# Kernel tuning notes

Hardware: AMD Instinct MI355X
Metric: run time of the kernel (lower is better)

## Reference

```python
import jax, jax.numpy as jnp
import numpy as np

N_NODES = 50000
N_EDGES = 800000
IN_C = 128
OUT_C = 128
ALPHA = 0.2  # leaky_relu negative slope (args.egat_alpha)
EDGE_K = 3   # edgefeat width, fixed by W_out in-dim = 3*out_channels


def setup_inputs() -> dict:
    key = jax.random.key(0)
    k = jax.random.split(key, 7)
    h = jax.random.normal(k[0], (N_NODES, IN_C), dtype=jnp.float32)
    edge_index = jax.random.randint(k[1], (2, N_EDGES), 0, N_NODES, dtype=jnp.int64)
    edgefeat = jax.random.uniform(k[2], (N_EDGES, EDGE_K), dtype=jnp.float32)
    # glorot-initialized linear weights (stored as [in, out] for x @ W)
    def glorot(kk, fan_in, fan_out):
        lim = jnp.sqrt(6.0 / (fan_in + fan_out)).astype(jnp.float32)
        return jax.random.uniform(kk, (fan_in, fan_out), jnp.float32, -lim, lim)
    W = glorot(k[3], IN_C, OUT_C)
    a1 = glorot(k[4], OUT_C, 1)
    a2 = glorot(k[5], OUT_C, 1)
    W_out = glorot(k[6], EDGE_K * OUT_C, OUT_C)
    return {"h": h, "edge_index": edge_index, "edgefeat": edgefeat,
            "W": W, "a1": a1, "a2": a2, "W_out": W_out}


def reference(h, edge_index, edgefeat, W, a1, a2, W_out):
    src = edge_index[0]  # j: message source
    dst = edge_index[1]  # i: aggregation target
    n = h.shape[0]

    Wh = h @ W                                   # [N, C]
    s1 = Wh @ a1                                 # [N, 1] alpha_j scores
    s2 = Wh @ a2                                 # [N, 1] alpha_i scores

    # edge_update: leaky_relu(alpha_j + alpha_i) * edge_attr, then edge softmax over dst
    e = s1[src] + s2[dst]                        # [E, 1]
    e = jnp.where(e >= 0, e, ALPHA * e)
    alpha = e * edgefeat                         # [E, 3]
    m = jax.ops.segment_max(alpha, dst, num_segments=n)      # [N, 3]
    m = jnp.where(jnp.isfinite(m), m, 0.0)
    ex = jnp.exp(alpha - m[dst])
    denom = jax.ops.segment_sum(ex, dst, num_segments=n)     # [N, 3]
    att = ex / (denom[dst] + 1e-16)              # [E, 3] (dropout p applied at eval -> identity)

    # message: outer product att[E,3] x x_j[E,C] -> [E, 3C] -> W_out -> [E, C]
    x_j = Wh[src]                                # [E, C]
    msg = (att[:, :, None] * x_j[:, None, :]).reshape(att.shape[0], EDGE_K * Wh.shape[1])
    msg = msg @ W_out                            # [E, C]

    # aggregate: sum at destination nodes
    out = jax.ops.segment_sum(msg, dst, num_segments=n)      # [N, C]
    return out
```

## Files before the change

kernel.cpp:

```cpp
#include <hip/hip_runtime.h>
#include <hip/hip_bf16.h>

#define ALPHA 0.2f
typedef unsigned int uint32;
typedef __attribute__((ext_vector_type(8))) short short8;
typedef __attribute__((ext_vector_type(4))) float f32x4;

static __device__ __forceinline__ unsigned short f2bf(float f) {
    unsigned int u = __float_as_uint(f);
    u += 0x7fffu + ((u >> 16) & 1u);
    return (unsigned short)(u >> 16);
}
static __device__ __forceinline__ uint32 pk2bf(float lo, float hi) {
    return (uint32)f2bf(lo) | ((uint32)f2bf(hi) << 16);
}
static __device__ __forceinline__ float bflo(uint32 u) { return __uint_as_float(u << 16); }
static __device__ __forceinline__ float bfhi(uint32 u) { return __uint_as_float(u & 0xffff0000u); }

__global__ __launch_bounds__(256) void k1_hist_prep(const int* __restrict__ ei,
                                                    int* __restrict__ counts,
                                                    int* __restrict__ eslot, int E,
                                                    const float* __restrict__ W,
                                                    const float* __restrict__ Wout,
                                                    const float* __restrict__ a1,
                                                    const float* __restrict__ a2,
                                                    unsigned short* __restrict__ WBT,
                                                    unsigned short* __restrict__ WoutT,
                                                    float* __restrict__ w1f,
                                                    float* __restrict__ w2f, int nbh) {
    const int tid = threadIdx.x;
    if ((int)blockIdx.x < nbh) {
        int e = blockIdx.x * 256 + tid;
        if (e < E) eslot[e] = atomicAdd(&counts[ei[E + e]], 1);
        return;
    }
    int bp = blockIdx.x - nbh;
    if (bp < 8) {
        for (int n = bp * 16; n < bp * 16 + 16; ++n)
            for (int c = tid; c < 128; c += 256)
                WBT[n * 128 + c] = f2bf(W[c * 128 + n]);
    } else if (bp < 24) {
        int q = bp - 8;
        for (int n = q * 8; n < q * 8 + 8; ++n)
            for (int c = tid; c < 384; c += 256)
                WoutT[n * 384 + c] = f2bf(Wout[c * 128 + n]);
    } else {
        if (tid < 128) {
            float acc1 = 0.f, acc2 = 0.f;
            for (int c = 0; c < 128; ++c) {
                float w = W[tid * 128 + c];
                acc1 += w * a1[c];
                acc2 += w * a2[c];
            }
            w1f[tid] = acc1;
            w2f[tid] = acc2;
        }
    }
}

__global__ __launch_bounds__(256) void k2_mmy_scan(const float* __restrict__ h,
                                                   const unsigned short* __restrict__ WBT,
                                                   const float* __restrict__ w1f,
                                                   const float* __restrict__ w2f,
                                                   unsigned short* __restrict__ Whb,
                                                   float* __restrict__ s1,
                                                   uint2* __restrict__ PR, int M,
                                                   const int* __restrict__ counts,
                                                   int* __restrict__ rowptr,
                                                   int N, int E, int nbm) {
    __shared__ unsigned short As[64 * 128];
    __shared__ unsigned short Bs[128 * 128];
    __shared__ float ws1[128], ws2[128];
    __shared__ int wsums[4];
    __shared__ int base_s;
    const int tid = threadIdx.x;

    if ((int)blockIdx.x >= nbm) {
        const int bs   = blockIdx.x - nbm;
        const int lane = tid & 63, wv = tid >> 6;
        const int limit = bs * 1024;
        int acc = 0;
        for (int i = tid * 4; i < limit; i += 1024) {
            int4 v = *(const int4*)(counts + i);
            acc += v.x + v.y + v.z + v.w;
        }
#pragma unroll
        for (int off = 32; off > 0; off >>= 1) acc += __shfl_down(acc, off);
        if (lane == 0) wsums[wv] = acc;
        __syncthreads();
        if (tid == 0) base_s = wsums[0] + wsums[1] + wsums[2] + wsums[3];
        __syncthreads();
        int i0 = bs * 1024 + tid * 4;
        int v0 = 0, v1 = 0, v2 = 0, v3 = 0;
        if (i0 + 3 < N) {
            int4 v = *(const int4*)(counts + i0);
            v0 = v.x; v1 = v.y; v2 = v.z; v3 = v.w;
        } else {
            if (i0 + 0 < N) v0 = counts[i0 + 0];
            if (i0 + 1 < N) v1 = counts[i0 + 1];
            if (i0 + 2 < N) v2 = counts[i0 + 2];
            if (i0 + 3 < N) v3 = counts[i0 + 3];
        }
        int tt = v0 + v1 + v2 + v3;
        int incl = tt;
#pragma unroll
        for (int off = 1; off < 64; off <<= 1) {
            int t = __shfl_up(incl, off);
            if (lane >= off) incl += t;
        }
        __syncthreads();
        if (lane == 63) wsums[wv] = incl;
        __syncthreads();
        int woff = 0;
        for (int w2 = 0; w2 < wv; ++w2) woff += wsums[w2];
        int base = base_s + woff + (incl - tt);
        if (i0 + 0 < N) { rowptr[i0 + 0] = base;                PR[i0 + 0].y = (uint32)base; }
        if (i0 + 1 < N) { rowptr[i0 + 1] = base + v0;           PR[i0 + 1].y = (uint32)(base + v0); }
        if (i0 + 2 < N) { rowptr[i0 + 2] = base + v0 + v1;      PR[i0 + 2].y = (uint32)(base + v0 + v1); }
        if (i0 + 3 < N) { rowptr[i0 + 3] = base + v0 + v1 + v2; PR[i0 + 3].y = (uint32)(base + v0 + v1 + v2); }
        if (bs == 0 && tid == 0) rowptr[N] = E;
        return;
    }

    const int lane = tid & 63;
    const int w    = tid >> 6;
    const int row0 = blockIdx.x * 64;

    if (tid < 128) ws1[tid] = w1f[tid];
    else           ws2[tid - 128] = w2f[tid - 128];
    __syncthreads();

    const float4* h4 = (const float4*)h;
    float sp1[4], sp2[4];
#pragma unroll
    for (int m = 0; m < 4; ++m) { sp1[m] = 0.f; sp2[m] = 0.f; }
#pragma unroll
    for (int m = 0; m < 4; ++m) {
        int i = m * 256 + tid;
        int r = i >> 4, g = i & 15;
        int rg = row0 + r;
        float4 va = make_float4(0.f, 0.f, 0.f, 0.f), vb = va;
        if (rg < M) {
            va = h4[(size_t)rg * 32 + g * 2];
            vb = h4[(size_t)rg * 32 + g * 2 + 1];
        }
        float4 wa1 = *(const float4*)(ws1 + g * 8);
        float4 wb1 = *(const float4*)(ws1 + g * 8 + 4);
        float4 wa2 = *(const float4*)(ws2 + g * 8);
        float4 wb2 = *(const float4*)(ws2 + g * 8 + 4);
        sp1[m] += va.x * wa1.x + va.y * wa1.y + va.z * wa1.z + va.w * wa1.w
                + vb.x * wb1.x + vb.y * wb1.y + vb.z * wb1.z + vb.w * wb1.w;
        sp2[m] += va.x * wa2.x + va.y * wa2.y + va.z * wa2.z + va.w * wa2.w
                + vb.x * wb2.x + vb.y * wb2.y + vb.z * wb2.z + vb.w * wb2.w;
        uint4 u;
        u.x = pk2bf(va.x, va.y); u.y = pk2bf(va.z, va.w);
        u.z = pk2bf(vb.x, vb.y); u.w = pk2bf(vb.z, vb.w);
        *(uint4*)(As + r * 128 + ((g ^ (r & 15)) * 8)) = u;
    }
#pragma unroll
    for (int m = 0; m < 4; ++m) {
#pragma unroll
        for (int off = 1; off < 16; off <<= 1) {
            sp1[m] += __shfl_xor(sp1[m], off);
            sp2[m] += __shfl_xor(sp2[m], off);
        }
    }
    if ((tid & 15) == 0) {
#pragma unroll
        for (int m = 0; m < 4; ++m) {
            int rg = row0 + m * 16 + (tid >> 4);
            if (rg < M) { s1[rg] = sp1[m]; PR[rg].x = __float_as_uint(sp2[m]); }
        }
    }

#pragma unroll
    for (int m = 0; m < 8; ++m) {
        int i = m * 256 + tid;
        int n = i >> 4, g = i & 15;
        uint4 v = *(const uint4*)(WBT + n * 128 + g * 8);
        *(uint4*)(Bs + n * 128 + ((g ^ (n & 15)) * 8)) = v;
    }
    __syncthreads();

    const int ml   = lane & 15;
    const int quad = lane >> 4;
    f32x4 acc[8];
#pragma unroll
    for (int nt = 0; nt < 8; ++nt) acc[nt] = (f32x4){0.f, 0.f, 0.f, 0.f};
#pragma unroll
    for (int kc = 0; kc < 4; ++kc) {
        int gl = ((kc * 4 + quad) ^ ml) * 8;
        short8 af = *(const short8*)(As + (w * 16 + ml) * 128 + gl);
#pragma unroll
        for (int nt = 0; nt < 8; ++nt) {
            short8 bf = *(const short8*)(Bs + (nt * 16 + ml) * 128 + gl);
            acc[nt] = __builtin_amdgcn_mfma_f32_16x16x32_bf16(af, bf, acc[nt], 0, 0, 0);
        }
    }
    __syncthreads();
    unsigned short* Ct = Bs;
    int lrow = w * 16 + quad * 4;
#pragma unroll
    for (int r = 0; r < 4; ++r)
#pragma unroll
        for (int nt = 0; nt < 8; ++nt)
            Ct[(lrow + r) * 136 + nt * 16 + ml] = f2bf(acc[nt][r]);
    __syncthreads();
#pragma unroll
    for (int m = 0; m < 4; ++m) {
        int i = m * 256 + tid;
        int r2 = i >> 4, g = i & 15;
        int rg = row0 + r2;
        uint4 v = *(const uint4*)(Ct + r2 * 136 + g * 8);
        if (rg < M)
            *(uint4*)(Whb + (size_t)rg * 128 + g * 8) = v;
    }
}

__global__ __launch_bounds__(256) void scatter_kernel(const int* __restrict__ ei,
                                                      const float* __restrict__ ef,
                                                      const float* __restrict__ s1,
                                                      const uint2* __restrict__ PR,
                                                      const int* __restrict__ eslot,
                                                      uint2* __restrict__ rec8, int E) {
    int e = blockIdx.x * blockDim.x + threadIdx.x;
    if (e >= E) return;
    int src = ei[e];
    int dst = ei[E + e];
    uint2 pr = PR[dst];
    float s = s1[src] + __uint_as_float(pr.x);
    s = (s >= 0.f) ? s : ALPHA * s;
    unsigned short b0 = f2bf(__expf(s * ef[e * 3 + 0]));
    unsigned short b1 = f2bf(__expf(s * ef[e * 3 + 1]));
    unsigned short b2 = f2bf(__expf(s * ef[e * 3 + 2]));
    uint2 rv;
    rv.x = (uint32)src | ((uint32)(b0 & 0x7fffu) << 17);
    rv.y = (uint32)(b1 & 0x7fffu) | ((uint32)(b2 & 0x7fffu) << 15);
    int pos = (int)pr.y + eslot[e];
    rec8[pos] = rv;
}

__global__ __launch_bounds__(256) void agg_kernel(const uint2* __restrict__ rec8,
                                                  const int* __restrict__ rowptr,
                                                  const uint32* __restrict__ Yu,
                                                  uint32* __restrict__ zo, int N) {
    int node = (blockIdx.x * blockDim.x + threadIdx.x) >> 6;
    int lane = threadIdx.x & 63;
    if (node >= N) return;
    int beg = rowptr[node], end = rowptr[node + 1];

    float d0 = 0.f, d1 = 0.f, d2 = 0.f;
    float z0l = 0.f, z0h = 0.f, z1l = 0.f, z1h = 0.f, z2l = 0.f, z2h = 0.f;
    int j = beg;

    for (; j + 7 < end; j += 8) {
        uint2 rr[8];
#pragma unroll
        for (int q = 0; q < 8; ++q) rr[q] = rec8[j + q];
        uint32 sx[8], sy[8];
#pragma unroll
        for (int q = 0; q < 8; ++q) {
            sx[q] = __builtin_amdgcn_readfirstlane(rr[q].x);
            sy[q] = __builtin_amdgcn_readfirstlane(rr[q].y);
        }
        uint32 u[8];
#pragma unroll
        for (int q = 0; q < 8; ++q)
            u[q] = Yu[(size_t)(sx[q] & 0x1ffffu) * 64 + lane];
#pragma unroll
        for (int q = 0; q < 8; ++q) {
            float w0 = __uint_as_float((sx[q] >> 1) & 0x7fff0000u);
            float w1 = __uint_as_float((sy[q] << 16) & 0x7fff0000u);
            float w2 = __uint_as_float((sy[q] << 1) & 0x7fff0000u);
            d0 += w0; d1 += w1; d2 += w2;
            float yl = bflo(u[q]), yh = bfhi(u[q]);
            z0l += w0 * yl; z0h += w0 * yh;
            z1l += w1 * yl; z1h += w1 * yh;
            z2l += w2 * yl; z2h += w2 * yh;
        }
    }
    for (; j + 3 < end; j += 4) {
        uint2 rr[4];
#pragma unroll
        for (int q = 0; q < 4; ++q) rr[q] = rec8[j + q];
        uint32 sx[4], sy[4];
#pragma unroll
        for (int q = 0; q < 4; ++q) {
            sx[q] = __builtin_amdgcn_readfirstlane(rr[q].x);
            sy[q] = __builtin_amdgcn_readfirstlane(rr[q].y);
        }
        uint32 u[4];
#pragma unroll
        for (int q = 0; q < 4; ++q)
            u[q] = Yu[(size_t)(sx[q] & 0x1ffffu) * 64 + lane];
#pragma unroll
        for (int q = 0; q < 4; ++q) {
            float w0 = __uint_as_float((sx[q] >> 1) & 0x7fff0000u);
            float w1 = __uint_as_float((sy[q] << 16) & 0x7fff0000u);
            float w2 = __uint_as_float((sy[q] << 1) & 0x7fff0000u);
            d0 += w0; d1 += w1; d2 += w2;
            float yl = bflo(u[q]), yh = bfhi(u[q]);
            z0l += w0 * yl; z0h += w0 * yh;
            z1l += w1 * yl; z1h += w1 * yh;
            z2l += w2 * yl; z2h += w2 * yh;
        }
    }
    for (; j < end; ++j) {
        uint2 r0 = rec8[j];
        uint32 sx = __builtin_amdgcn_readfirstlane(r0.x);
        uint32 sy = __builtin_amdgcn_readfirstlane(r0.y);
        uint32 u0 = Yu[(size_t)(sx & 0x1ffffu) * 64 + lane];
        float w0 = __uint_as_float((sx >> 1) & 0x7fff0000u);
        float w1 = __uint_as_float((sy << 16) & 0x7fff0000u);
        float w2 = __uint_as_float((sy << 1) & 0x7fff0000u);
        d0 += w0; d1 += w1; d2 += w2;
        float yl = bflo(u0), yh = bfhi(u0);
        z0l += w0 * yl; z0h += w0 * yh;
        z1l += w1 * yl; z1h += w1 * yh;
        z2l += w2 * yl; z2h += w2 * yh;
    }
    float i0 = 1.f / (d0 + 1e-16f);
    float i1 = 1.f / (d1 + 1e-16f);
    float i2 = 1.f / (d2 + 1e-16f);
    size_t zb = (size_t)node * 192;
    zo[zb + lane]       = pk2bf(z0l * i0, z0h * i0);
    zo[zb + 64 + lane]  = pk2bf(z1l * i1, z1h * i1);
    zo[zb + 128 + lane] = pk2bf(z2l * i2, z2h * i2);
}

__global__ __launch_bounds__(256) void k5_gemm(const unsigned short* __restrict__ z,
                                               const unsigned short* __restrict__ WoutT,
                                               float* __restrict__ out, int M) {
    __shared__ __align__(16) char smem[49152];
    unsigned short* As = (unsigned short*)smem;
    unsigned short* Bs = (unsigned short*)(smem + 16384);
    float* Ct = (float*)smem;
    const int tid = threadIdx.x;
    const int lane = tid & 63, w = tid >> 6;
    const int ml = lane & 15, quad = lane >> 4;
    const int row0 = blockIdx.x * 64;

    f32x4 acc[8];
#pragma unroll
    for (int nt = 0; nt < 8; ++nt) acc[nt] = (f32x4){0.f, 0.f, 0.f, 0.f};

    for (int ks = 0; ks < 3; ++ks) {
        __syncthreads();
#pragma unroll
        for (int m = 0; m < 4; ++m) {
            int i = m * 256 + tid;
            int r = i >> 4, g = i & 15;
            int rg = row0 + r;
            uint4 v = make_uint4(0u, 0u, 0u, 0u);
            if (rg < M) v = *(const uint4*)(z + (size_t)rg * 384 + ks * 128 + g * 8);
            *(uint4*)(As + r * 128 + ((g ^ (r & 15)) * 8)) = v;
        }
#pragma unroll
        for (int m = 0; m < 8; ++m) {
            int i = m * 256 + tid;
            int n = i >> 4, g = i & 15;
            uint4 v = *(const uint4*)(WoutT + n * 384 + ks * 128 + g * 8);
            *(uint4*)(Bs + n * 128 + ((g ^ (n & 15)) * 8)) = v;
        }
        __syncthreads();
#pragma unroll
        for (int kc = 0; kc < 4; ++kc) {
            int gl = ((kc * 4 + quad) ^ ml) * 8;
            short8 af = *(const short8*)(As + (w * 16 + ml) * 128 + gl);
#pragma unroll
            for (int nt = 0; nt < 8; ++nt) {
                short8 bf = *(const short8*)(Bs + (nt * 16 + ml) * 128 + gl);
                acc[nt] = __builtin_amdgcn_mfma_f32_16x16x32_bf16(af, bf, acc[nt], 0, 0, 0);
            }
        }
    }
    __syncthreads();
    int lrow = w * 16 + quad * 4;
#pragma unroll
    for (int r = 0; r < 4; ++r)
#pragma unroll
        for (int nt = 0; nt < 8; ++nt)
            Ct[(lrow + r) * 132 + nt * 16 + ml] = acc[nt][r];
    __syncthreads();
#pragma unroll
    for (int m = 0; m < 8; ++m) {
        int i = m * 256 + tid;
        int r2 = i >> 5, g = i & 31;
        int rg = row0 + r2;
        if (rg < M)
            *(float4*)(out + (size_t)rg * 128 + g * 4) = *(const float4*)(Ct + r2 * 132 + g * 4);
    }
}

extern "C" void kernel_launch(void* const* d_in, const int* in_sizes, int n_in,
                              void* d_out, int out_size, void* d_ws, size_t ws_size,
                              hipStream_t stream) {
    const float* h    = (const float*)d_in[0];
    const int*   ei   = (const int*)d_in[1];
    const float* ef   = (const float*)d_in[2];
    const float* W    = (const float*)d_in[3];
    const float* a1   = (const float*)d_in[4];
    const float* a2   = (const float*)d_in[5];
    const float* Wout = (const float*)d_in[6];
    float*       out  = (float*)d_out;

    const int N = in_sizes[0] / 128;
    const int E = in_sizes[2] / 3;
    const int nchunk = (N + 1023) / 1024;
    const int nbh    = (E + 255) / 256;
    const int nbm    = (N + 63) / 64;

    uint2* rec8 = (uint2*)d_ws;
    unsigned short* Whb = (unsigned short*)(rec8 + E);
    unsigned short* WBT = Whb + (size_t)N * 128;
    unsigned short* WoutT = WBT + 128 * 128;
    float* w1f  = (float*)(WoutT + 128 * 384);
    float* w2f  = w1f + 128;
    float* s1   = w2f + 128;
    uint2* PR   = (uint2*)(s1 + N);
    int* rowptr = (int*)(PR + N);
    unsigned short* zbuf = (unsigned short*)(rowptr + N + 4);
    int* counts = (int*)zbuf;
    int* eslot  = counts + N;

    (void)hipMemsetAsync(counts, 0, (size_t)N * sizeof(int), stream);

    k1_hist_prep<<<nbh + 25, 256, 0, stream>>>(ei, counts, eslot, E,
                                               W, Wout, a1, a2, WBT, WoutT, w1f, w2f, nbh);
    k2_mmy_scan<<<nbm + nchunk, 256, 0, stream>>>(h, WBT, w1f, w2f, Whb, s1, PR, N,
                                                  counts, rowptr, N, E, nbm);
    scatter_kernel<<<(E + 255) / 256, 256, 0, stream>>>(ei, ef, s1, PR, eslot, rec8, E);
    agg_kernel<<<(N * 64 + 255) / 256, 256, 0, stream>>>(rec8, rowptr, (const uint32*)Whb,
                                                         (uint32*)zbuf, N);
    k5_gemm<<<(N + 63) / 64, 256, 0, stream>>>(zbuf, WoutT, out, N);
}
```

Before: 217.2 us.

## Fuse aggregation with Wout GEMM and replace eslot with scatter-time atomics

```diff
diff --git a/kernel.cpp b/kernel.cpp
--- a/kernel.cpp
+++ b/kernel.cpp
@@ -18,8 +18,7 @@
 static __device__ __forceinline__ float bfhi(uint32 u) { return __uint_as_float(u & 0xffff0000u); }
 
 __global__ __launch_bounds__(256) void k1_hist_prep(const int* __restrict__ ei,
-                                                    int* __restrict__ counts,
-                                                    int* __restrict__ eslot, int E,
+                                                    int* __restrict__ counts, int E,
                                                     const float* __restrict__ W,
                                                     const float* __restrict__ Wout,
                                                     const float* __restrict__ a1,
@@ -30,8 +29,16 @@
                                                     float* __restrict__ w2f, int nbh) {
     const int tid = threadIdx.x;
     if ((int)blockIdx.x < nbh) {
-        int e = blockIdx.x * 256 + tid;
-        if (e < E) eslot[e] = atomicAdd(&counts[ei[E + e]], 1);
+        int e0 = (blockIdx.x * 256 + tid) * 4;
+        if (e0 + 3 < E) {
+            int4 d = *(const int4*)(ei + E + e0);
+            atomicAdd(&counts[d.x], 1);
+            atomicAdd(&counts[d.y], 1);
+            atomicAdd(&counts[d.z], 1);
+            atomicAdd(&counts[d.w], 1);
+        } else {
+            for (int e = e0; e < E; ++e) atomicAdd(&counts[ei[E + e]], 1);
+        }
         return;
     }
     int bp = blockIdx.x - nbh;
@@ -220,15 +227,13 @@
 __global__ __launch_bounds__(256) void scatter_kernel(const int* __restrict__ ei,
                                                       const float* __restrict__ ef,
                                                       const float* __restrict__ s1,
-                                                      const uint2* __restrict__ PR,
-                                                      const int* __restrict__ eslot,
+                                                      uint2* PR,
                                                       uint2* __restrict__ rec8, int E) {
     int e = blockIdx.x * blockDim.x + threadIdx.x;
     if (e >= E) return;
     int src = ei[e];
     int dst = ei[E + e];
-    uint2 pr = PR[dst];
-    float s = s1[src] + __uint_as_float(pr.x);
+    float s = s1[src] + __uint_as_float(((const uint32*)PR)[2 * (size_t)dst]);
     s = (s >= 0.f) ? s : ALPHA * s;
     unsigned short b0 = f2bf(__expf(s * ef[e * 3 + 0]));
     unsigned short b1 = f2bf(__expf(s * ef[e * 3 + 1]));
@@ -236,159 +241,144 @@
     uint2 rv;
     rv.x = (uint32)src | ((uint32)(b0 & 0x7fffu) << 17);
     rv.y = (uint32)(b1 & 0x7fffu) | ((uint32)(b2 & 0x7fffu) << 15);
-    int pos = (int)pr.y + eslot[e];
+    int pos = atomicAdd((int*)((uint32*)PR + 2 * (size_t)dst + 1), 1);
     rec8[pos] = rv;
 }
 
-__global__ __launch_bounds__(256) void agg_kernel(const uint2* __restrict__ rec8,
-                                                  const int* __restrict__ rowptr,
-                                                  const uint32* __restrict__ Yu,
-                                                  uint32* __restrict__ zo, int N) {
-    int node = (blockIdx.x * blockDim.x + threadIdx.x) >> 6;
-    int lane = threadIdx.x & 63;
-    if (node >= N) return;
-    int beg = rowptr[node], end = rowptr[node + 1];
-
-    float d0 = 0.f, d1 = 0.f, d2 = 0.f;
-    float z0l = 0.f, z0h = 0.f, z1l = 0.f, z1h = 0.f, z2l = 0.f, z2h = 0.f;
-    int j = beg;
-
-    for (; j + 7 < end; j += 8) {
-        uint2 rr[8];
-#pragma unroll
-        for (int q = 0; q < 8; ++q) rr[q] = rec8[j + q];
-        uint32 sx[8], sy[8];
-#pragma unroll
-        for (int q = 0; q < 8; ++q) {
-            sx[q] = __builtin_amdgcn_readfirstlane(rr[q].x);
-            sy[q] = __builtin_amdgcn_readfirstlane(rr[q].y);
-        }
-        uint32 u[8];
-#pragma unroll
-        for (int q = 0; q < 8; ++q)
-            u[q] = Yu[(size_t)(sx[q] & 0x1ffffu) * 64 + lane];
-#pragma unroll
-        for (int q = 0; q < 8; ++q) {
-            float w0 = __uint_as_float((sx[q] >> 1) & 0x7fff0000u);
-            float w1 = __uint_as_float((sy[q] << 16) & 0x7fff0000u);
-            float w2 = __uint_as_float((sy[q] << 1) & 0x7fff0000u);
+__global__ __launch_bounds__(256) void agg_fused(const uint2* __restrict__ rec8,
+                                                 const int* __restrict__ rowptr,
+                                                 const uint32* __restrict__ Yu,
+                                                 const unsigned short* __restrict__ WoutT,
+                                                 float* __restrict__ out, int N) {
+    __shared__ uint32 zs32[16 * 192];
+    const int tid  = threadIdx.x;
+    const int lane = tid & 63, w = tid >> 6;
+    const int ml   = lane & 15, quad = lane >> 4;
+    const int nb   = blockIdx.x * 16;
+
+#pragma unroll
+    for (int rnd = 0; rnd < 4; ++rnd) {
+        int r    = rnd * 4 + w;
+        int node = nb + r;
+        if (node >= N) continue;
+        int beg = rowptr[node], end = rowptr[node + 1];
+
+        float d0 = 0.f, d1 = 0.f, d2 = 0.f;
+        float z0l = 0.f, z0h = 0.f, z1l = 0.f, z1h = 0.f, z2l = 0.f, z2h = 0.f;
+        int j = beg;
+        for (; j + 7 < end; j += 8) {
+            uint2 rr[8];
+#pragma unroll
+            for (int q = 0; q < 8; ++q) rr[q] = rec8[j + q];
+            uint32 sx[8], sy[8];
+#pragma unroll
+            for (int q = 0; q < 8; ++q) {
+                sx[q] = __builtin_amdgcn_readfirstlane(rr[q].x);
+                sy[q] = __builtin_amdgcn_readfirstlane(rr[q].y);
+            }
+            uint32 u[8];
+#pragma unroll
+            for (int q = 0; q < 8; ++q)
+                u[q] = Yu[(size_t)(sx[q] & 0x1ffffu) * 64 + lane];
+#pragma unroll
+            for (int q = 0; q < 8; ++q) {
+                float w0 = __uint_as_float((sx[q] >> 1) & 0x7fff0000u);
+                float w1 = __uint_as_float((sy[q] << 16) & 0x7fff0000u);
+                float w2 = __uint_as_float((sy[q] << 1) & 0x7fff0000u);
+                d0 += w0; d1 += w1; d2 += w2;
+                float yl = bflo(u[q]), yh = bfhi(u[q]);
+                z0l += w0 * yl; z0h += w0 * yh;
+                z1l += w1 * yl; z1h += w1 * yh;
+                z2l += w2 * yl; z2h += w2 * yh;
+            }
+        }
+        for (; j + 3 < end; j += 4) {
+            uint2 rr[4];
+#pragma unroll
+            for (int q = 0; q < 4; ++q) rr[q] = rec8[j + q];
+            uint32 sx[4], sy[4];
+#pragma unroll
+            for (int q = 0; q < 4; ++q) {
+                sx[q] = __builtin_amdgcn_readfirstlane(rr[q].x);
+                sy[q] = __builtin_amdgcn_readfirstlane(rr[q].y);
+            }
+            uint32 u[4];
+#pragma unroll
+            for (int q = 0; q < 4; ++q)
+                u[q] = Yu[(size_t)(sx[q] & 0x1ffffu) * 64 + lane];
+#pragma unroll
+            for (int q = 0; q < 4; ++q) {
+                float w0 = __uint_as_float((sx[q] >> 1) & 0x7fff0000u);
+                float w1 = __uint_as_float((sy[q] << 16) & 0x7fff0000u);
+                float w2 = __uint_as_float((sy[q] << 1) & 0x7fff0000u);
+                d0 += w0; d1 += w1; d2 += w2;
+                float yl = bflo(u[q]), yh = bfhi(u[q]);
+                z0l += w0 * yl; z0h += w0 * yh;
+                z1l += w1 * yl; z1h += w1 * yh;
+                z2l += w2 * yl; z2h += w2 * yh;
+            }
+        }
+        for (; j < end; ++j) {
+            uint2 r0 = rec8[j];
+            uint32 sx = __builtin_amdgcn_readfirstlane(r0.x);
+            uint32 sy = __builtin_amdgcn_readfirstlane(r0.y);
+            uint32 u0 = Yu[(size_t)(sx & 0x1ffffu) * 64 + lane];
+            float w0 = __uint_as_float((sx >> 1) & 0x7fff0000u);
+            float w1 = __uint_as_float((sy << 16) & 0x7fff0000u);
+            float w2 = __uint_as_float((sy << 1) & 0x7fff0000u);
             d0 += w0; d1 += w1; d2 += w2;
-            float yl = bflo(u[q]), yh = bfhi(u[q]);
+            float yl = bflo(u0), yh = bfhi(u0);
             z0l += w0 * yl; z0h += w0 * yh;
             z1l += w1 * yl; z1h += w1 * yh;
             z2l += w2 * yl; z2h += w2 * yh;
         }
-    }
-    for (; j + 3 < end; j += 4) {
-        uint2 rr[4];
-#pragma unroll
-        for (int q = 0; q < 4; ++q) rr[q] = rec8[j + q];
-        uint32 sx[4], sy[4];
-#pragma unroll
-        for (int q = 0; q < 4; ++q) {
-            sx[q] = __builtin_amdgcn_readfirstlane(rr[q].x);
-            sy[q] = __builtin_amdgcn_readfirstlane(rr[q].y);
-        }
-        uint32 u[4];
-#pragma unroll
-        for (int q = 0; q < 4; ++q)
-            u[q] = Yu[(size_t)(sx[q] & 0x1ffffu) * 64 + lane];
-#pragma unroll
-        for (int q = 0; q < 4; ++q) {
-            float w0 = __uint_as_float((sx[q] >> 1) & 0x7fff0000u);
-            float w1 = __uint_as_float((sy[q] << 16) & 0x7fff0000u);
-            float w2 = __uint_as_float((sy[q] << 1) & 0x7fff0000u);
-            d0 += w0; d1 += w1; d2 += w2;
-            float yl = bflo(u[q]), yh = bfhi(u[q]);
-            z0l += w0 * yl; z0h += w0 * yh;
-            z1l += w1 * yl; z1h += w1 * yh;
-            z2l += w2 * yl; z2h += w2 * yh;
-        }
-    }
-    for (; j < end; ++j) {
-        uint2 r0 = rec8[j];
-        uint32 sx = __builtin_amdgcn_readfirstlane(r0.x);
-        uint32 sy = __builtin_amdgcn_readfirstlane(r0.y);
-        uint32 u0 = Yu[(size_t)(sx & 0x1ffffu) * 64 + lane];
-        float w0 = __uint_as_float((sx >> 1) & 0x7fff0000u);
-        float w1 = __uint_as_float((sy << 16) & 0x7fff0000u);
-        float w2 = __uint_as_float((sy << 1) & 0x7fff0000u);
-        d0 += w0; d1 += w1; d2 += w2;
-        float yl = bflo(u0), yh = bfhi(u0);
-        z0l += w0 * yl; z0h += w0 * yh;
-        z1l += w1 * yl; z1h += w1 * yh;
-        z2l += w2 * yl; z2h += w2 * yh;
-    }
-    float i0 = 1.f / (d0 + 1e-16f);
-    float i1 = 1.f / (d1 + 1e-16f);
-    float i2 = 1.f / (d2 + 1e-16f);
-    size_t zb = (size_t)node * 192;
-    zo[zb + lane]       = pk2bf(z0l * i0, z0h * i0);
-    zo[zb + 64 + lane]  = pk2bf(z1l * i1, z1h * i1);
-    zo[zb + 128 + lane] = pk2bf(z2l * i2, z2h * i2);
-}
-
-__global__ __launch_bounds__(256) void k5_gemm(const unsigned short* __restrict__ z,
-                                               const unsigned short* __restrict__ WoutT,
-                                               float* __restrict__ out, int M) {
-    __shared__ __align__(16) char smem[49152];
-    unsigned short* As = (unsigned short*)smem;
-    unsigned short* Bs = (unsigned short*)(smem + 16384);
-    float* Ct = (float*)smem;
-    const int tid = threadIdx.x;
-    const int lane = tid & 63, w = tid >> 6;
-    const int ml = lane & 15, quad = lane >> 4;
-    const int row0 = blockIdx.x * 64;
-
-    f32x4 acc[8];
-#pragma unroll
-    for (int nt = 0; nt < 8; ++nt) acc[nt] = (f32x4){0.f, 0.f, 0.f, 0.f};
-
-    for (int ks = 0; ks < 3; ++ks) {
-        __syncthreads();
-#pragma unroll
-        for (int m = 0; m < 4; ++m) {
-            int i = m * 256 + tid;
-            int r = i >> 4, g = i & 15;
-            int rg = row0 + r;
-            uint4 v = make_uint4(0u, 0u, 0u, 0u);
-            if (rg < M) v = *(const uint4*)(z + (size_t)rg * 384 + ks * 128 + g * 8);
-            *(uint4*)(As + r * 128 + ((g ^ (r & 15)) * 8)) = v;
-        }
-#pragma unroll
-        for (int m = 0; m < 8; ++m) {
-            int i = m * 256 + tid;
-            int n = i >> 4, g = i & 15;
-            uint4 v = *(const uint4*)(WoutT + n * 384 + ks * 128 + g * 8);
-            *(uint4*)(Bs + n * 128 + ((g ^ (n & 15)) * 8)) = v;
-        }
-        __syncthreads();
-#pragma unroll
-        for (int kc = 0; kc < 4; ++kc) {
-            int gl = ((kc * 4 + quad) ^ ml) * 8;
-            short8 af = *(const short8*)(As + (w * 16 + ml) * 128 + gl);
-#pragma unroll
-            for (int nt = 0; nt < 8; ++nt) {
-                short8 bf = *(const short8*)(Bs + (nt * 16 + ml) * 128 + gl);
-                acc[nt] = __builtin_amdgcn_mfma_f32_16x16x32_bf16(af, bf, acc[nt], 0, 0, 0);
-            }
-        }
-    }
-    __syncthreads();
-    int lrow = w * 16 + quad * 4;
+        float i0 = 1.f / (d0 + 1e-16f);
+        float i1 = 1.f / (d1 + 1e-16f);
+        float i2 = 1.f / (d2 + 1e-16f);
+        uint32 zp[3] = { pk2bf(z0l * i0, z0h * i0),
+                         pk2bf(z1l * i1, z1h * i1),
+                         pk2bf(z2l * i2, z2h * i2) };
+#pragma unroll
+        for (int k = 0; k < 3; ++k) {
+            int g  = k * 16 + (lane >> 2);
+            int sg = (g & ~7) | ((g ^ r) & 7);
+            zs32[r * 192 + sg * 4 + (lane & 3)] = zp[k];
+        }
+    }
+    __syncthreads();
+
+    const int n0 = w * 32;
+    f32x4 acc[2];
+    acc[0] = (f32x4){0.f, 0.f, 0.f, 0.f};
+    acc[1] = (f32x4){0.f, 0.f, 0.f, 0.f};
+    const unsigned short* zs16 = (const unsigned short*)zs32;
+#pragma unroll
+    for (int ks = 0; ks < 12; ++ks) {
+        int g  = ks * 4 + quad;
+        int sg = (g & ~7) | ((g ^ ml) & 7);
+        short8 af = *(const short8*)(zs16 + ml * 384 + sg * 8);
+#pragma unroll
+        for (int nt = 0; nt < 2; ++nt) {
+            short8 bf = *(const short8*)(WoutT + (size_t)(n0 + nt * 16 + ml) * 384
+                                         + ks * 32 + quad * 8);
+            acc[nt] = __builtin_amdgcn_mfma_f32_16x16x32_bf16(af, bf, acc[nt], 0, 0, 0);
+        }
+    }
+    __syncthreads();
+    float* Ct = (float*)zs32;
 #pragma unroll
     for (int r = 0; r < 4; ++r)
 #pragma unroll
-        for (int nt = 0; nt < 8; ++nt)
-            Ct[(lrow + r) * 132 + nt * 16 + ml] = acc[nt][r];
-    __syncthreads();
-#pragma unroll
-    for (int m = 0; m < 8; ++m) {
-        int i = m * 256 + tid;
-        int r2 = i >> 5, g = i & 31;
-        int rg = row0 + r2;
-        if (rg < M)
-            *(float4*)(out + (size_t)rg * 128 + g * 4) = *(const float4*)(Ct + r2 * 132 + g * 4);
+        for (int nt = 0; nt < 2; ++nt)
+            Ct[(quad * 4 + r) * 132 + n0 + nt * 16 + ml] = acc[nt][r];
+    __syncthreads();
+#pragma unroll
+    for (int m = 0; m < 2; ++m) {
+        int i   = m * 256 + tid;
+        int row = i >> 5, g = i & 31;
+        int node = nb + row;
+        if (node < N)
+            *(float4*)(out + (size_t)node * 128 + g * 4) = *(const float4*)(Ct + row * 132 + g * 4);
     }
 }
 
@@ -407,7 +397,7 @@
     const int N = in_sizes[0] / 128;
     const int E = in_sizes[2] / 3;
     const int nchunk = (N + 1023) / 1024;
-    const int nbh    = (E + 255) / 256;
+    const int nbh    = (E + 1023) / 1024;
     const int nbm    = (N + 63) / 64;
 
     uint2* rec8 = (uint2*)d_ws;
@@ -419,18 +409,15 @@
     float* s1   = w2f + 128;
     uint2* PR   = (uint2*)(s1 + N);
     int* rowptr = (int*)(PR + N);
-    unsigned short* zbuf = (unsigned short*)(rowptr + N + 4);
-    int* counts = (int*)zbuf;
-    int* eslot  = counts + N;
+    int* counts = rowptr + N + 4;
 
     (void)hipMemsetAsync(counts, 0, (size_t)N * sizeof(int), stream);
 
-    k1_hist_prep<<<nbh + 25, 256, 0, stream>>>(ei, counts, eslot, E,
+    k1_hist_prep<<<nbh + 25, 256, 0, stream>>>(ei, counts, E,
                                                W, Wout, a1, a2, WBT, WoutT, w1f, w2f, nbh);
     k2_mmy_scan<<<nbm + nchunk, 256, 0, stream>>>(h, WBT, w1f, w2f, Whb, s1, PR, N,
                                                   counts, rowptr, N, E, nbm);
-    scatter_kernel<<<(E + 255) / 256, 256, 0, stream>>>(ei, ef, s1, PR, eslot, rec8, E);
-    agg_kernel<<<(N * 64 + 255) / 256, 256, 0, stream>>>(rec8, rowptr, (const uint32*)Whb,
-                                                         (uint32*)zbuf, N);
-    k5_gemm<<<(N + 63) / 64, 256, 0, stream>>>(zbuf, WoutT, out, N);
-}
+    scatter_kernel<<<(E + 255) / 256, 256, 0, stream>>>(ei, ef, s1, PR, rec8, E);
+    agg_fused<<<(N + 15) / 16, 256, 0, stream>>>(rec8, rowptr, (const uint32*)Whb,
+                                                 WoutT, out, N);
+}
```

New measurement: 320.1 us. 1.47x slower.

## Vectorize edge histogram and scatter, prefetch records in aggregation loop

Applied to the files above, without the earlier changes.

```diff
diff --git a/kernel.cpp b/kernel.cpp
--- a/kernel.cpp
+++ b/kernel.cpp
@@ -30,8 +30,20 @@
                                                     float* __restrict__ w2f, int nbh) {
     const int tid = threadIdx.x;
     if ((int)blockIdx.x < nbh) {
-        int e = blockIdx.x * 256 + tid;
-        if (e < E) eslot[e] = atomicAdd(&counts[ei[E + e]], 1);
+        int e0 = (blockIdx.x * 256 + tid) * 4;
+        if (e0 + 3 < E) {
+            int4 d = *(const int4*)(ei + E + e0);
+            int s0 = atomicAdd(&counts[d.x], 1);
+            int s1v = atomicAdd(&counts[d.y], 1);
+            int s2v = atomicAdd(&counts[d.z], 1);
+            int s3 = atomicAdd(&counts[d.w], 1);
+            eslot[e0]     = s0;
+            eslot[e0 + 1] = s1v;
+            eslot[e0 + 2] = s2v;
+            eslot[e0 + 3] = s3;
+        } else {
+            for (int e = e0; e < E; ++e) eslot[e] = atomicAdd(&counts[ei[E + e]], 1);
+        }
         return;
     }
     int bp = blockIdx.x - nbh;
@@ -223,21 +235,58 @@
                                                       const uint2* __restrict__ PR,
                                                       const int* __restrict__ eslot,
                                                       uint2* __restrict__ rec8, int E) {
-    int e = blockIdx.x * blockDim.x + threadIdx.x;
-    if (e >= E) return;
-    int src = ei[e];
-    int dst = ei[E + e];
-    uint2 pr = PR[dst];
-    float s = s1[src] + __uint_as_float(pr.x);
-    s = (s >= 0.f) ? s : ALPHA * s;
-    unsigned short b0 = f2bf(__expf(s * ef[e * 3 + 0]));
-    unsigned short b1 = f2bf(__expf(s * ef[e * 3 + 1]));
-    unsigned short b2 = f2bf(__expf(s * ef[e * 3 + 2]));
-    uint2 rv;
-    rv.x = (uint32)src | ((uint32)(b0 & 0x7fffu) << 17);
-    rv.y = (uint32)(b1 & 0x7fffu) | ((uint32)(b2 & 0x7fffu) << 15);
-    int pos = (int)pr.y + eslot[e];
-    rec8[pos] = rv;
+    int e0 = (blockIdx.x * blockDim.x + threadIdx.x) * 4;
+    if (e0 >= E) return;
+    if (e0 + 3 < E) {
+        int4 sv = *(const int4*)(ei + e0);
+        int4 dv = *(const int4*)(ei + E + e0);
+        int4 es = *(const int4*)(eslot + e0);
+        float4 f0 = *(const float4*)(ef + (size_t)e0 * 3);
+        float4 f1 = *(const float4*)(ef + (size_t)e0 * 3 + 4);
+        float4 f2 = *(const float4*)(ef + (size_t)e0 * 3 + 8);
+        float sa = s1[sv.x], sb = s1[sv.y], sc = s1[sv.z], sd = s1[sv.w];
+        uint2 pa = PR[dv.x], pb = PR[dv.y], pc = PR[dv.z], pd = PR[dv.w];
+        float s_a = sa + __uint_as_float(pa.x);
+        float s_b = sb + __uint_as_float(pb.x);
+        float s_c = sc + __uint_as_float(pc.x);
+        float s_d = sd + __uint_as_float(pd.x);
+        s_a = (s_a >= 0.f) ? s_a : ALPHA * s_a;
+        s_b = (s_b >= 0.f) ? s_b : ALPHA * s_b;
+        s_c = (s_c >= 0.f) ? s_c : ALPHA * s_c;
+        s_d = (s_d >= 0.f) ? s_d : ALPHA * s_d;
+        uint2 rv;
+        rv.x = (uint32)sv.x | ((uint32)(f2bf(__expf(s_a * f0.x)) & 0x7fffu) << 17);
+        rv.y = (uint32)(f2bf(__expf(s_a * f0.y)) & 0x7fffu)
+             | ((uint32)(f2bf(__expf(s_a * f0.z)) & 0x7fffu) << 15);
+        rec8[(int)pa.y + es.x] = rv;
+        rv.x = (uint32)sv.y | ((uint32)(f2bf(__expf(s_b * f0.w)) & 0x7fffu) << 17);
+        rv.y = (uint32)(f2bf(__expf(s_b * f1.x)) & 0x7fffu)
+             | ((uint32)(f2bf(__expf(s_b * f1.y)) & 0x7fffu) << 15);
+        rec8[(int)pb.y + es.y] = rv;
+        rv.x = (uint32)sv.z | ((uint32)(f2bf(__expf(s_c * f1.z)) & 0x7fffu) << 17);
+        rv.y = (uint32)(f2bf(__expf(s_c * f1.w)) & 0x7fffu)
+             | ((uint32)(f2bf(__expf(s_c * f2.x)) & 0x7fffu) << 15);
+        rec8[(int)pc.y + es.z] = rv;
+        rv.x = (uint32)sv.w | ((uint32)(f2bf(__expf(s_d * f2.y)) & 0x7fffu) << 17);
+        rv.y = (uint32)(f2bf(__expf(s_d * f2.z)) & 0x7fffu)
+             | ((uint32)(f2bf(__expf(s_d * f2.w)) & 0x7fffu) << 15);
+        rec8[(int)pd.y + es.w] = rv;
+    } else {
+        for (int e = e0; e < E; ++e) {
+            int src = ei[e];
+            int dst = ei[E + e];
+            uint2 pr = PR[dst];
+            float s = s1[src] + __uint_as_float(pr.x);
+            s = (s >= 0.f) ? s : ALPHA * s;
+            unsigned short b0 = f2bf(__expf(s * ef[(size_t)e * 3 + 0]));
+            unsigned short b1 = f2bf(__expf(s * ef[(size_t)e * 3 + 1]));
+            unsigned short b2 = f2bf(__expf(s * ef[(size_t)e * 3 + 2]));
+            uint2 rv;
+            rv.x = (uint32)src | ((uint32)(b0 & 0x7fffu) << 17);
+            rv.y = (uint32)(b1 & 0x7fffu) | ((uint32)(b2 & 0x7fffu) << 15);
+            rec8[(int)pr.y + eslot[e]] = rv;
+        }
+    }
 }
 
 __global__ __launch_bounds__(256) void agg_kernel(const uint2* __restrict__ rec8,
@@ -247,16 +296,20 @@
     int node = (blockIdx.x * blockDim.x + threadIdx.x) >> 6;
     int lane = threadIdx.x & 63;
     if (node >= N) return;
-    int beg = rowptr[node], end = rowptr[node + 1];
+    int nu  = __builtin_amdgcn_readfirstlane(node);
+    int beg = rowptr[nu], end = rowptr[nu + 1];
 
     float d0 = 0.f, d1 = 0.f, d2 = 0.f;
     float z0l = 0.f, z0h = 0.f, z1l = 0.f, z1h = 0.f, z2l = 0.f, z2h = 0.f;
     int j = beg;
 
-    for (; j + 7 < end; j += 8) {
-        uint2 rr[8];
-#pragma unroll
-        for (int q = 0; q < 8; ++q) rr[q] = rec8[j + q];
+    uint2 rr[8];
+    if (j + 7 < end) {
+        const uint2* rb = rec8 + (unsigned)__builtin_amdgcn_readfirstlane(j);
+#pragma unroll
+        for (int q = 0; q < 8; ++q) rr[q] = rb[q];
+    }
+    while (j + 7 < end) {
         uint32 sx[8], sy[8];
 #pragma unroll
         for (int q = 0; q < 8; ++q) {
@@ -267,6 +320,12 @@
 #pragma unroll
         for (int q = 0; q < 8; ++q)
             u[q] = Yu[(size_t)(sx[q] & 0x1ffffu) * 64 + lane];
+        int jn = j + 8;
+        if (jn + 7 < end) {
+            const uint2* rb = rec8 + (unsigned)__builtin_amdgcn_readfirstlane(jn);
+#pragma unroll
+            for (int q = 0; q < 8; ++q) rr[q] = rb[q];
+        }
 #pragma unroll
         for (int q = 0; q < 8; ++q) {
             float w0 = __uint_as_float((sx[q] >> 1) & 0x7fff0000u);
@@ -278,16 +337,18 @@
             z1l += w1 * yl; z1h += w1 * yh;
             z2l += w2 * yl; z2h += w2 * yh;
         }
+        j = jn;
     }
     for (; j + 3 < end; j += 4) {
-        uint2 rr[4];
-#pragma unroll
-        for (int q = 0; q < 4; ++q) rr[q] = rec8[j + q];
+        const uint2* rb = rec8 + (unsigned)__builtin_amdgcn_readfirstlane(j);
+        uint2 r4[4];
+#pragma unroll
+        for (int q = 0; q < 4; ++q) r4[q] = rb[q];
         uint32 sx[4], sy[4];
 #pragma unroll
         for (int q = 0; q < 4; ++q) {
-            sx[q] = __builtin_amdgcn_readfirstlane(rr[q].x);
-            sy[q] = __builtin_amdgcn_readfirstlane(rr[q].y);
+            sx[q] = __builtin_amdgcn_readfirstlane(r4[q].x);
+            sy[q] = __builtin_amdgcn_readfirstlane(r4[q].y);
         }
         uint32 u[4];
 #pragma unroll
@@ -306,7 +367,8 @@
         }
     }
     for (; j < end; ++j) {
-        uint2 r0 = rec8[j];
+        const uint2* rb = rec8 + (unsigned)__builtin_amdgcn_readfirstlane(j);
+        uint2 r0 = rb[0];
         uint32 sx = __builtin_amdgcn_readfirstlane(r0.x);
         uint32 sy = __builtin_amdgcn_readfirstlane(r0.y);
         uint32 u0 = Yu[(size_t)(sx & 0x1ffffu) * 64 + lane];
@@ -407,7 +469,7 @@
     const int N = in_sizes[0] / 128;
     const int E = in_sizes[2] / 3;
     const int nchunk = (N + 1023) / 1024;
-    const int nbh    = (E + 255) / 256;
+    const int nbh    = (E + 1023) / 1024;
     const int nbm    = (N + 63) / 64;
 
     uint2* rec8 = (uint2*)d_ws;
@@ -429,7 +491,7 @@
                                                W, Wout, a1, a2, WBT, WoutT, w1f, w2f, nbh);
     k2_mmy_scan<<<nbm + nchunk, 256, 0, stream>>>(h, WBT, w1f, w2f, Whb, s1, PR, N,
                                                   counts, rowptr, N, E, nbm);
-    scatter_kernel<<<(E + 255) / 256, 256, 0, stream>>>(ei, ef, s1, PR, eslot, rec8, E);
+    scatter_kernel<<<(E / 4 + 255) / 256, 256, 0, stream>>>(ei, ef, s1, PR, eslot, rec8, E);
     agg_kernel<<<(N * 64 + 255) / 256, 256, 0, stream>>>(rec8, rowptr, (const uint32*)Whb,
                                                          (uint32*)zbuf, N);
     k5_gemm<<<(N + 63) / 64, 256, 0, stream>>>(zbuf, WoutT, out, N);
```

Result: no change. 213.2 us, median of 2 (-1.9%).
